# Kernel optimization log

Measured on AMD Instinct MI355X. Metric: run time of the kernel, lower is better.

## Reference

```python
import jax, jax.numpy as jnp
import numpy as np

EMB = 384
HEADS = 6
QDIM = 64
DFF = 4 * EMB
EPS = 1e-5


def layer_norm(x, g, b):
    mu = jnp.mean(x, axis=-1, keepdims=True)
    var = jnp.mean((x - mu) ** 2, axis=-1, keepdims=True)
    return (x - mu) * jax.lax.rsqrt(var + EPS) * g + b


def setup_inputs() -> dict:
    key = jax.random.key(0)
    ks = jax.random.split(key, 12)
    s = EMB ** -0.5
    return {
        "x": jax.random.normal(ks[0], (32, 512, EMB), dtype=jnp.float32),
        "Wq": jax.random.normal(ks[1], (EMB, EMB), dtype=jnp.float32) * s,
        "Wk": jax.random.normal(ks[2], (EMB, EMB), dtype=jnp.float32) * s,
        "Wv": jax.random.normal(ks[3], (EMB, EMB), dtype=jnp.float32) * s,
        "Wp": jax.random.normal(ks[4], (EMB, EMB), dtype=jnp.float32) * s,
        "bp": jnp.zeros((EMB,), dtype=jnp.float32),
        "g1": jnp.ones((EMB,), dtype=jnp.float32),
        "b1": jnp.zeros((EMB,), dtype=jnp.float32),
        "g2": jnp.ones((EMB,), dtype=jnp.float32),
        "b2": jnp.zeros((EMB,), dtype=jnp.float32),
        "W1": jax.random.normal(ks[5], (EMB, DFF), dtype=jnp.float32) * s,
        "bf1": jnp.zeros((DFF,), dtype=jnp.float32),
        "W2": jax.random.normal(ks[6], (DFF, EMB), dtype=jnp.float32) * (DFF ** -0.5),
        "bf2": jnp.zeros((EMB,), dtype=jnp.float32),
    }


def reference(x, Wq, Wk, Wv, Wp, bp, g1, b1, g2, b2, W1, bf1, W2, bf2):
    B, T, C = x.shape
    # --- self-attention on ln1(x) ---
    h = layer_norm(x, g1, b1)
    q = (h @ Wq).reshape(B, T, HEADS, QDIM).transpose(0, 2, 1, 3)  # [B,H,T,D]
    k = (h @ Wk).reshape(B, T, HEADS, QDIM).transpose(0, 2, 1, 3)
    v = (h @ Wv).reshape(B, T, HEADS, QDIM).transpose(0, 2, 1, 3)
    aff = jnp.einsum('bhtd,bhsd->bhts', q, k) * (QDIM ** -0.5)  # [B,H,T,T]
    causal = jnp.tril(jnp.ones((T, T), dtype=bool))
    aff = jnp.where(causal, aff, -jnp.inf)
    aff = jax.nn.softmax(aff, axis=-1)
    o = jnp.einsum('bhts,bhsd->bhtd', aff, v)
    o = o.transpose(0, 2, 1, 3).reshape(B, T, C)
    x = x + (o @ Wp + bp)
    # --- feed-forward on ln2(x) ---
    h2 = layer_norm(x, g2, b2)
    ff = jax.nn.relu(h2 @ W1 + bf1) @ W2 + bf2
    return x + ff
```

## Files before the change

kernel.cpp:

```cpp
#include <hip/hip_runtime.h>
#include <cstdint>
#include <cstddef>

#define DEVINL __device__ __forceinline__

typedef short short8 __attribute__((ext_vector_type(8)));
typedef float f32x4 __attribute__((ext_vector_type(4)));
typedef unsigned short ushort;
typedef ushort u16x8 __attribute__((ext_vector_type(8)));
typedef ushort u16x4 __attribute__((ext_vector_type(4)));

DEVINL float bf2f(ushort u) {
  union { unsigned int i; float f; } v; v.i = ((unsigned int)u) << 16; return v.f;
}
DEVINL ushort f2bf(float f) {
  union { float f; unsigned int i; } v; v.f = f;
  unsigned int u = v.i;
  unsigned int r = u + 0x7fffu + ((u >> 16) & 1u);
  return (ushort)(r >> 16);
}

DEVINL void gl2lds16(const ushort* g, ushort* l) {
  __builtin_amdgcn_global_load_lds(
      (const __attribute__((address_space(1))) void*)g,
      (__attribute__((address_space(3))) void*)l, 16, 0, 0);
}

__global__ void transpose6_k(const float* __restrict__ Wq, const float* __restrict__ Wk,
                             const float* __restrict__ Wv, const float* __restrict__ Wp,
                             const float* __restrict__ W1, const float* __restrict__ W2,
                             ushort* __restrict__ WqT, ushort* __restrict__ WkT,
                             ushort* __restrict__ WvT, ushort* __restrict__ WpT,
                             ushort* __restrict__ W1T, ushort* __restrict__ W2T) {
  __shared__ float tile[32][33];
  int z = blockIdx.z;
  const float* in;
  ushort* out;
  int R, C, bx, by;
  if (z < 4) {
    if (blockIdx.x >= 12) return;
    in = (z == 0) ? Wq : (z == 1) ? Wk : (z == 2) ? Wv : Wp;
    out = (z == 0) ? WqT : (z == 1) ? WkT : (z == 2) ? WvT : WpT;
    R = 384; C = 384; bx = blockIdx.x; by = blockIdx.y;
  } else if (z == 4) {
    in = W1; out = W1T; R = 384; C = 1536; bx = blockIdx.x; by = blockIdx.y;
  } else {
    in = W2; out = W2T; R = 1536; C = 384; bx = blockIdx.y; by = blockIdx.x;
  }
  int tx = threadIdx.x, ty = threadIdx.y;
  int x = bx * 32 + tx;
#pragma unroll
  for (int i = 0; i < 4; i++) {
    int y = by * 32 + ty + i * 8;
    tile[ty + i * 8][tx] = in[(size_t)y * C + x];
  }
  __syncthreads();
  int x2 = by * 32 + tx;
#pragma unroll
  for (int i = 0; i < 4; i++) {
    int y2 = bx * 32 + ty + i * 8;
    out[(size_t)y2 * R + x2] = f2bf(tile[tx][ty + i * 8]);
  }
}

__global__ __launch_bounds__(256) void ln_k(const float* __restrict__ x,
                                            const float* __restrict__ g,
                                            const float* __restrict__ b,
                                            ushort* __restrict__ out) {
  int wave = threadIdx.x >> 6;
  int lane = threadIdx.x & 63;
  int row = blockIdx.x * 4 + wave;
  const float* xr = x + (size_t)row * 384;
  float v[6];
#pragma unroll
  for (int j = 0; j < 3; j++) {
    float2 p = *(const float2*)(xr + lane * 2 + j * 128);
    v[2 * j] = p.x;
    v[2 * j + 1] = p.y;
  }
  float s = v[0] + v[1] + v[2] + v[3] + v[4] + v[5];
#pragma unroll
  for (int off = 32; off; off >>= 1) s += __shfl_xor(s, off);
  float mu = s * (1.0f / 384.0f);
  float s2 = 0.f;
#pragma unroll
  for (int j = 0; j < 6; j++) { float d = v[j] - mu; s2 += d * d; }
#pragma unroll
  for (int off = 32; off; off >>= 1) s2 += __shfl_xor(s2, off);
  float rs = rsqrtf(s2 * (1.0f / 384.0f) + 1e-5f);
  ushort* orow = out + (size_t)row * 384;
#pragma unroll
  for (int j = 0; j < 3; j++) {
    int c = lane * 2 + j * 128;
    float2 pg = *(const float2*)(g + c);
    float2 pb = *(const float2*)(b + c);
    float y0 = (v[2 * j] - mu) * rs * pg.x + pb.x;
    float y1 = (v[2 * j + 1] - mu) * rs * pg.y + pb.y;
    uint32_t po = (uint32_t)f2bf(y0) | ((uint32_t)f2bf(y1) << 16);
    *(uint32_t*)(orow + c) = po;
  }
}

template <int MODE, int TN>
__global__ __launch_bounds__(256) void gemm_k(
    const ushort* __restrict__ A, int K,
    const ushort* __restrict__ WTa, const ushort* __restrict__ WTb,
    const ushort* __restrict__ WTc,
    const float* __restrict__ bias,
    ushort* __restrict__ outa, ushort* __restrict__ outb,
    ushort* __restrict__ outc) {
  constexpr int NJ = TN / 32;
  __shared__ __align__(16) ushort As[128 * 64];
  __shared__ __align__(16) ushort Bs[TN * 64];
  int tid = threadIdx.x;
  int lane = tid & 63, wave = tid >> 6;
  int wm = wave & 1, wn = wave >> 1;
  int q4 = lane >> 4, ln16 = lane & 15;
  int rowBase = blockIdx.x * 128;
  int colBase = blockIdx.y * TN;

  const ushort* WT;
  if (MODE == 0) {
    int z = blockIdx.z;
    WT = (z == 0) ? WTa : (z == 1) ? WTb : WTc;
  } else {
    WT = WTa;
  }

  f32x4 acc[4][NJ];
#pragma unroll
  for (int i = 0; i < 4; i++)
#pragma unroll
    for (int j = 0; j < NJ; j++) acc[i][j] = (f32x4){0.f, 0.f, 0.f, 0.f};

  int ri = lane >> 3;
  int g8 = (lane & 7) ^ ri;

  for (int kb = 0; kb < K; kb += 64) {
#pragma unroll
    for (int h = 0; h < 128; h += 32) {
      int base = h + wave * 8;
      gl2lds16(&A[(size_t)(rowBase + base + ri) * K + kb + g8 * 8], &As[base * 64]);
    }
#pragma unroll
    for (int h = 0; h < TN; h += 32) {
      int base = h + wave * 8;
      gl2lds16(&WT[(size_t)(colBase + base + ri) * K + kb + g8 * 8], &Bs[base * 64]);
    }
    __syncthreads();
#pragma unroll
    for (int ks = 0; ks < 2; ks++) {
      short8 af[4], bfr[NJ];
#pragma unroll
      for (int i = 0; i < 4; i++) {
        int ar = wm * 64 + i * 16 + ln16;
        int slot = (ks * 4 + q4) ^ (ar & 7);
        af[i] = *(const short8*)&As[ar * 64 + slot * 8];
      }
#pragma unroll
      for (int j = 0; j < NJ; j++) {
        int br = wn * (TN / 2) + j * 16 + ln16;
        int slot = (ks * 4 + q4) ^ (br & 7);
        bfr[j] = *(const short8*)&Bs[br * 64 + slot * 8];
      }
#pragma unroll
      for (int i = 0; i < 4; i++)
#pragma unroll
        for (int j = 0; j < NJ; j++)
          acc[i][j] = __builtin_amdgcn_mfma_f32_16x16x32_bf16(af[i], bfr[j], acc[i][j], 0, 0, 0);
    }
    __syncthreads();
  }

#pragma unroll
  for (int i = 0; i < 4; i++) {
#pragma unroll
    for (int j = 0; j < NJ; j++) {
      int row0 = rowBase + wm * 64 + i * 16 + q4 * 4;
      int col = colBase + wn * (TN / 2) + j * 16 + ln16;
      if (MODE == 0) {
        int z = blockIdx.z;
        if (z < 2) {
          float sc = (z == 0) ? 0.18033688011112f : 1.0f;
          ushort* o = (z == 0) ? outa : outb;
#pragma unroll
          for (int r = 0; r < 4; r++) {
            int row = row0 + r;
            int bb = row >> 9, t = row & 511, h = col >> 6, d = col & 63;
            o[(((size_t)(bb * 6 + h) * 512) + t) * 64 + d] = f2bf(acc[i][j][r] * sc);
          }
        } else {
          int bb = row0 >> 9, t0 = row0 & 511, h = col >> 6, d = col & 63;
          u16x4 pk = {f2bf(acc[i][j][0]), f2bf(acc[i][j][1]), f2bf(acc[i][j][2]),
                      f2bf(acc[i][j][3])};
          *(u16x4*)&outc[(((size_t)(bb * 6 + h) * 64) + d) * 512 + t0] = pk;
        }
      } else {
        float bcol = bias[col];
#pragma unroll
        for (int r = 0; r < 4; r++) {
          size_t idx = (size_t)(row0 + r) * 1536 + col;
          float vv = acc[i][j][r] + bcol;
          outa[idx] = f2bf(vv > 0.f ? vv : 0.f);
        }
      }
    }
  }
}

template <int EPI>
__global__ __launch_bounds__(512, 4) void gemmrow_k(
    const ushort* __restrict__ A, int K, const ushort* __restrict__ WT,
    const float* __restrict__ bias, const float* __restrict__ residf,
    const float* __restrict__ g, const float* __restrict__ bln,
    float* __restrict__ outf, ushort* __restrict__ outh) {
  __shared__ __align__(16) ushort As[64 * 64];
  __shared__ __align__(16) ushort Bs[384 * 64];
  int tid = threadIdx.x;
  int lane = tid & 63, wave = tid >> 6;
  int wm = wave & 1, wn = wave >> 1;
  int q4 = lane >> 4, ln16 = lane & 15;
  int rowBase = blockIdx.x * 64;

  f32x4 acc[2][6];
#pragma unroll
  for (int i = 0; i < 2; i++)
#pragma unroll
    for (int j = 0; j < 6; j++) acc[i][j] = (f32x4){0.f, 0.f, 0.f, 0.f};

  int ri = lane >> 3;
  int g8 = (lane & 7) ^ ri;

  for (int kb = 0; kb < K; kb += 64) {
    gl2lds16(&A[(size_t)(rowBase + wave * 8 + ri) * K + kb + g8 * 8],
             &As[(wave * 8) * 64]);
#pragma unroll
    for (int s = 0; s < 6; s++) {
      int base = s * 64 + wave * 8;
      gl2lds16(&WT[(size_t)(base + ri) * K + kb + g8 * 8], &Bs[base * 64]);
    }
    __syncthreads();
#pragma unroll
    for (int ks = 0; ks < 2; ks++) {
      short8 af[2], bfr[6];
#pragma unroll
      for (int i = 0; i < 2; i++) {
        int ar = wm * 32 + i * 16 + ln16;
        int slot = (ks * 4 + q4) ^ (ar & 7);
        af[i] = *(const short8*)&As[ar * 64 + slot * 8];
      }
#pragma unroll
      for (int j = 0; j < 6; j++) {
        int br = wn * 96 + j * 16 + ln16;
        int slot = (ks * 4 + q4) ^ (br & 7);
        bfr[j] = *(const short8*)&Bs[br * 64 + slot * 8];
      }
#pragma unroll
      for (int i = 0; i < 2; i++)
#pragma unroll
        for (int j = 0; j < 6; j++)
          acc[i][j] = __builtin_amdgcn_mfma_f32_16x16x32_bf16(af[i], bfr[j], acc[i][j], 0, 0, 0);
    }
    __syncthreads();
  }

  float s1[2][4], s2v[2][4];
#pragma unroll
  for (int i = 0; i < 2; i++)
#pragma unroll
    for (int r = 0; r < 4; r++) { s1[i][r] = 0.f; s2v[i][r] = 0.f; }

#pragma unroll
  for (int i = 0; i < 2; i++) {
#pragma unroll
    for (int j = 0; j < 6; j++) {
      int col = wn * 96 + j * 16 + ln16;
      float bcol = bias[col];
      int row0 = rowBase + wm * 32 + i * 16 + q4 * 4;
#pragma unroll
      for (int r = 0; r < 4; r++) {
        size_t idx = (size_t)(row0 + r) * 384 + col;
        float val = acc[i][j][r] + bcol + residf[idx];
        outf[idx] = val;
        acc[i][j][r] = val;
        if (EPI == 0) { s1[i][r] += val; s2v[i][r] += val * val; }
      }
    }
  }

  if (EPI == 0) {
    float* red = (float*)As;
#pragma unroll
    for (int i = 0; i < 2; i++)
#pragma unroll
      for (int r = 0; r < 4; r++) {
        float a = s1[i][r], b = s2v[i][r];
#pragma unroll
        for (int m = 1; m <= 8; m <<= 1) {
          a += __shfl_xor(a, m);
          b += __shfl_xor(b, m);
        }
        if (ln16 == 0) {
          int lr = wm * 32 + i * 16 + q4 * 4 + r;
          red[wn * 64 + lr] = a;
          red[256 + wn * 64 + lr] = b;
        }
      }
    __syncthreads();
#pragma unroll
    for (int i = 0; i < 2; i++) {
#pragma unroll
      for (int r = 0; r < 4; r++) {
        int lr = wm * 32 + i * 16 + q4 * 4 + r;
        float a = red[lr] + red[64 + lr] + red[128 + lr] + red[192 + lr];
        float b = red[256 + lr] + red[320 + lr] + red[448 - 64 + lr] + red[448 + lr];
        float mu = a * (1.0f / 384.0f);
        float var = b * (1.0f / 384.0f) - mu * mu;
        float rs = rsqrtf(var + 1e-5f);
        int row = rowBase + lr;
#pragma unroll
        for (int j = 0; j < 6; j++) {
          int col = wn * 96 + j * 16 + ln16;
          float hv = (acc[i][j][r] - mu) * rs * g[col] + bln[col];
          outh[(size_t)row * 384 + col] = f2bf(hv);
        }
      }
    }
  }
}

__global__ __launch_bounds__(256) void attn_k(const ushort* __restrict__ qg,
                                              const ushort* __restrict__ kg,
                                              const ushort* __restrict__ vtg,
                                              ushort* __restrict__ outg) {
  __shared__ __align__(16) ushort Ks[64 * 64];
  __shared__ __align__(16) ushort VTs[64 * 64];
  __shared__ __align__(16) ushort Pw[4][16][88];
  int tid = threadIdx.x, lane = tid & 63, wave = tid >> 6;
  int l = blockIdx.x;
  int xcd = l & 7, m = l >> 3;
  int bh = xcd * 24 + (m >> 2);
  int pr = m & 3;
  int lo = pr, hi = 7 - pr;
  int quad = lane >> 4, ln16 = lane & 15;
  int x7 = ln16 & 7;
  int slo = (quad ^ x7) * 8;
  int shi = slo ^ 32;

  const ushort* qp = qg + (size_t)bh * 512 * 64;
  const ushort* kp = kg + (size_t)bh * 512 * 64;
  const ushort* vp = vtg + (size_t)bh * 64 * 512;

  int ri = lane >> 3;
  int g8 = (lane & 7) ^ ri;

  int t_lo = lo * 64 + wave * 16 + ln16;
  int t_hi = hi * 64 + wave * 16 + ln16;
  short8 bqlo0 = *(const short8*)&qp[(size_t)t_lo * 64 + quad * 8];
  short8 bqlo1 = *(const short8*)&qp[(size_t)t_lo * 64 + 32 + quad * 8];
  short8 bqhi0 = *(const short8*)&qp[(size_t)t_hi * 64 + quad * 8];
  short8 bqhi1 = *(const short8*)&qp[(size_t)t_hi * 64 + 32 + quad * 8];

  f32x4 Olo[4], Ohi[4];
#pragma unroll
  for (int dt = 0; dt < 4; dt++) {
    Olo[dt] = (f32x4){0.f, 0.f, 0.f, 0.f};
    Ohi[dt] = (f32x4){0.f, 0.f, 0.f, 0.f};
  }
  float m_lo = -3.0e38f, l_lo = 0.f, m_hi = -3.0e38f, l_hi = 0.f;

  auto process = [&](short8 q0f, short8 q1f, int t_row, float& m_, float& l_,
                     f32x4* O, int s0, bool maskit) {
    f32x4 St[4];
    __builtin_amdgcn_s_setprio(1);
#pragma unroll
    for (int kt = 0; kt < 4; kt++) {
      int r = kt * 16 + ln16;
      short8 a0 = *(const short8*)&Ks[r * 64 + slo];
      short8 a1 = *(const short8*)&Ks[r * 64 + shi];
      f32x4 z = (f32x4){0.f, 0.f, 0.f, 0.f};
      z = __builtin_amdgcn_mfma_f32_16x16x32_bf16(a0, q0f, z, 0, 0, 0);
      z = __builtin_amdgcn_mfma_f32_16x16x32_bf16(a1, q1f, z, 0, 0, 0);
      St[kt] = z;
    }
    __builtin_amdgcn_s_setprio(0);
    if (maskit) {
#pragma unroll
      for (int kt = 0; kt < 4; kt++)
#pragma unroll
        for (int r = 0; r < 4; r++) {
          int s_abs = s0 + kt * 16 + quad * 4 + r;
          St[kt][r] = (s_abs <= t_row) ? St[kt][r] : -3.0e38f;
        }
    }
    float vm = St[0][0];
#pragma unroll
    for (int kt = 0; kt < 4; kt++)
#pragma unroll
      for (int r = 0; r < 4; r++) vm = fmaxf(vm, St[kt][r]);
    vm = fmaxf(vm, __shfl_xor(vm, 16));
    vm = fmaxf(vm, __shfl_xor(vm, 32));
    float mn = fmaxf(m_, vm);
    if (!__all(mn - m_ <= 8.0f)) {
      float alpha = exp2f(m_ - mn);
      m_ = mn;
      l_ *= alpha;
#pragma unroll
      for (int dt = 0; dt < 4; dt++)
#pragma unroll
        for (int r = 0; r < 4; r++) O[dt][r] *= alpha;
    }
    float ps = 0.f;
#pragma unroll
    for (int kt = 0; kt < 4; kt++)
#pragma unroll
      for (int r = 0; r < 4; r++) {
        float p = exp2f(St[kt][r] - m_);
        St[kt][r] = p;
        ps += p;
      }
    ps += __shfl_xor(ps, 16);
    ps += __shfl_xor(ps, 32);
    l_ += ps;

    asm volatile("" ::: "memory");
#pragma unroll
    for (int kt = 0; kt < 4; kt++) {
      u16x4 pk = {f2bf(St[kt][0]), f2bf(St[kt][1]), f2bf(St[kt][2]), f2bf(St[kt][3])};
      *(u16x4*)&Pw[wave][ln16][kt * 16 + quad * 4] = pk;
    }
    asm volatile("" ::: "memory");
    union { u16x8 u; short8 s; } p0, p1;
    p0.u = *(const u16x8*)&Pw[wave][ln16][quad * 8];
    p1.u = *(const u16x8*)&Pw[wave][ln16][32 + quad * 8];
    __builtin_amdgcn_s_setprio(1);
#pragma unroll
    for (int dt = 0; dt < 4; dt++) {
      int r = dt * 16 + ln16;
      short8 v0 = *(const short8*)&VTs[r * 64 + slo];
      short8 v1 = *(const short8*)&VTs[r * 64 + shi];
      O[dt] = __builtin_amdgcn_mfma_f32_16x16x32_bf16(v0, p0.s, O[dt], 0, 0, 0);
      O[dt] = __builtin_amdgcn_mfma_f32_16x16x32_bf16(v1, p1.s, O[dt], 0, 0, 0);
    }
    __builtin_amdgcn_s_setprio(0);
  };

  for (int s0 = 0; s0 <= hi * 64; s0 += 64) {
#pragma unroll
    for (int h = 0; h < 64; h += 32) {
      int base = h + wave * 8;
      gl2lds16(&kp[(size_t)(s0 + base + ri) * 64 + g8 * 8], &Ks[base * 64]);
      gl2lds16(&vp[(size_t)(base + ri) * 512 + s0 + g8 * 8], &VTs[base * 64]);
    }
    __syncthreads();
    if (s0 <= lo * 64) process(bqlo0, bqlo1, t_lo, m_lo, l_lo, Olo, s0, s0 == lo * 64);
    process(bqhi0, bqhi1, t_hi, m_hi, l_hi, Ohi, s0, s0 == hi * 64);
    __syncthreads();
  }

  int b = bh / 6, h = bh % 6;
  float ilo = 1.0f / l_lo, ihi = 1.0f / l_hi;
  size_t base_lo = ((size_t)(b * 512) + t_lo) * 384 + h * 64;
  size_t base_hi = ((size_t)(b * 512) + t_hi) * 384 + h * 64;
#pragma unroll
  for (int dt = 0; dt < 4; dt++) {
    u16x4 plo = {f2bf(Olo[dt][0] * ilo), f2bf(Olo[dt][1] * ilo),
                 f2bf(Olo[dt][2] * ilo), f2bf(Olo[dt][3] * ilo)};
    *(u16x4*)&outg[base_lo + dt * 16 + quad * 4] = plo;
    u16x4 phi = {f2bf(Ohi[dt][0] * ihi), f2bf(Ohi[dt][1] * ihi),
                 f2bf(Ohi[dt][2] * ihi), f2bf(Ohi[dt][3] * ihi)};
    *(u16x4*)&outg[base_hi + dt * 16 + quad * 4] = phi;
  }
}

extern "C" void kernel_launch(void* const* d_in, const int* in_sizes, int n_in,
                              void* d_out, int out_size, void* d_ws, size_t ws_size,
                              hipStream_t stream) {
  const float* x = (const float*)d_in[0];
  const float* Wq = (const float*)d_in[1];
  const float* Wk = (const float*)d_in[2];
  const float* Wv = (const float*)d_in[3];
  const float* Wp = (const float*)d_in[4];
  const float* bp = (const float*)d_in[5];
  const float* g1 = (const float*)d_in[6];
  const float* b1 = (const float*)d_in[7];
  const float* g2 = (const float*)d_in[8];
  const float* b2 = (const float*)d_in[9];
  const float* W1 = (const float*)d_in[10];
  const float* bf1 = (const float*)d_in[11];
  const float* W2 = (const float*)d_in[12];
  const float* bf2 = (const float*)d_in[13];
  float* outp = (float*)d_out;

  char* ws = (char*)d_ws;
  size_t off = 0;
  auto alloc = [&](size_t elems) {
    ushort* p = (ushort*)(ws + off);
    off += elems * 2;
    return p;
  };
  ushort* WqT = alloc((size_t)384 * 384);
  ushort* WkT = alloc((size_t)384 * 384);
  ushort* WvT = alloc((size_t)384 * 384);
  ushort* WpT = alloc((size_t)384 * 384);
  ushort* W1T = alloc((size_t)384 * 1536);
  ushort* W2T = alloc((size_t)1536 * 384);
  ushort* bufq = alloc((size_t)16384 * 384);
  ushort* m1 = alloc((size_t)16384 * 1536);
  ushort* h1_attn = m1;
  ushort* bufk = m1 + (size_t)16384 * 384;
  ushort* vT = m1 + (size_t)2 * 16384 * 384;

  dim3 tb(32, 8);
  transpose6_k<<<dim3(48, 12, 6), tb, 0, stream>>>(Wq, Wk, Wv, Wp, W1, W2,
                                                   WqT, WkT, WvT, WpT, W1T, W2T);

  ln_k<<<4096, 256, 0, stream>>>(x, g1, b1, h1_attn);
  gemm_k<0, 128><<<dim3(128, 3, 3), 256, 0, stream>>>(
      h1_attn, 384, WqT, WkT, WvT, nullptr, bufq, bufk, vT);
  attn_k<<<768, 256, 0, stream>>>(bufq, bufk, vT, h1_attn);
  gemmrow_k<0><<<256, 512, 0, stream>>>(
      h1_attn, 384, WpT, bp, x, g2, b2, outp, bufq);
  gemm_k<2, 128><<<dim3(128, 12), 256, 0, stream>>>(
      bufq, 384, W1T, nullptr, nullptr, bf1, m1, nullptr, nullptr);
  gemmrow_k<1><<<256, 512, 0, stream>>>(
      m1, 1536, W2T, bf2, outp, nullptr, nullptr, outp, nullptr);
}
```

Before: 255.8 us.

## Double-buffer LDS tiles in row GEMM to overlap loads with MFMA

Converts the full-row GEMM kernel (Wp projection and FFN down-projection with fused residual and LayerNorm epilogue) to a two-stage LDS pipeline. It prefetches the next K tile via global_load_lds while computing on the current one, using one barrier per iteration instead of two. LDS use roughly doubles (about 112KB per block), so the occupancy hint drops from 4 to 2 blocks and at most one block may fit per CU. This trades occupancy-based latency hiding for explicit overlap.

```diff
diff --git a/kernel.cpp b/kernel.cpp
--- a/kernel.cpp
+++ b/kernel.cpp
@@ -209,13 +209,13 @@
 }
 
 template <int EPI>
-__global__ __launch_bounds__(512, 4) void gemmrow_k(
+__global__ __launch_bounds__(512, 2) void gemmrow_k(
     const ushort* __restrict__ A, int K, const ushort* __restrict__ WT,
     const float* __restrict__ bias, const float* __restrict__ residf,
     const float* __restrict__ g, const float* __restrict__ bln,
     float* __restrict__ outf, ushort* __restrict__ outh) {
-  __shared__ __align__(16) ushort As[64 * 64];
-  __shared__ __align__(16) ushort Bs[384 * 64];
+  __shared__ __align__(16) ushort As[2][64 * 64];
+  __shared__ __align__(16) ushort Bs[2][384 * 64];
   int tid = threadIdx.x;
   int lane = tid & 63, wave = tid >> 6;
   int wm = wave & 1, wn = wave >> 1;
@@ -231,15 +231,25 @@
   int ri = lane >> 3;
   int g8 = (lane & 7) ^ ri;
 
-  for (int kb = 0; kb < K; kb += 64) {
+  auto STAGE = [&](int buf, int kb) {
     gl2lds16(&A[(size_t)(rowBase + wave * 8 + ri) * K + kb + g8 * 8],
-             &As[(wave * 8) * 64]);
+             &As[buf][(wave * 8) * 64]);
 #pragma unroll
     for (int s = 0; s < 6; s++) {
       int base = s * 64 + wave * 8;
-      gl2lds16(&WT[(size_t)(base + ri) * K + kb + g8 * 8], &Bs[base * 64]);
-    }
-    __syncthreads();
+      gl2lds16(&WT[(size_t)(base + ri) * K + kb + g8 * 8], &Bs[buf][base * 64]);
+    }
+  };
+
+  int nt = K >> 6;
+  STAGE(0, 0);
+  asm volatile("s_waitcnt vmcnt(0)" ::: "memory");
+  __builtin_amdgcn_sched_barrier(0);
+  __builtin_amdgcn_s_barrier();
+
+  for (int t = 0; t < nt; ++t) {
+    int cur = t & 1;
+    if (t + 1 < nt) STAGE(cur ^ 1, (t + 1) << 6);
 #pragma unroll
     for (int ks = 0; ks < 2; ks++) {
       short8 af[2], bfr[6];
@@ -247,13 +257,13 @@
       for (int i = 0; i < 2; i++) {
         int ar = wm * 32 + i * 16 + ln16;
         int slot = (ks * 4 + q4) ^ (ar & 7);
-        af[i] = *(const short8*)&As[ar * 64 + slot * 8];
+        af[i] = *(const short8*)&As[cur][ar * 64 + slot * 8];
       }
 #pragma unroll
       for (int j = 0; j < 6; j++) {
         int br = wn * 96 + j * 16 + ln16;
         int slot = (ks * 4 + q4) ^ (br & 7);
-        bfr[j] = *(const short8*)&Bs[br * 64 + slot * 8];
+        bfr[j] = *(const short8*)&Bs[cur][br * 64 + slot * 8];
       }
 #pragma unroll
       for (int i = 0; i < 2; i++)
@@ -261,7 +271,10 @@
         for (int j = 0; j < 6; j++)
           acc[i][j] = __builtin_amdgcn_mfma_f32_16x16x32_bf16(af[i], bfr[j], acc[i][j], 0, 0, 0);
     }
-    __syncthreads();
+    __builtin_amdgcn_sched_barrier(0);
+    asm volatile("s_waitcnt vmcnt(0)" ::: "memory");
+    __builtin_amdgcn_sched_barrier(0);
+    __builtin_amdgcn_s_barrier();
   }
 
   float s1[2][4], s2v[2][4];
@@ -289,7 +302,7 @@
   }
 
   if (EPI == 0) {
-    float* red = (float*)As;
+    float* red = (float*)&As[0][0];
 #pragma unroll
     for (int i = 0; i < 2; i++)
 #pragma unroll
@@ -313,7 +326,7 @@
       for (int r = 0; r < 4; r++) {
         int lr = wm * 32 + i * 16 + q4 * 4 + r;
         float a = red[lr] + red[64 + lr] + red[128 + lr] + red[192 + lr];
-        float b = red[256 + lr] + red[320 + lr] + red[448 - 64 + lr] + red[448 + lr];
+        float b = red[256 + lr] + red[320 + lr] + red[384 + lr] + red[448 + lr];
         float mu = a * (1.0f / 384.0f);
         float var = b * (1.0f / 384.0f) - mu * mu;
         float rs = rsqrtf(var + 1e-5f);
```

Measured after the change: 248.4 us. 2.9% less time.
